# Kernel optimization log

Hardware: AMD Instinct MI355X
Metric: run time of the kernel (lower is better)

Reference implementation:

```python
import jax, jax.numpy as jnp
import numpy as np

B, IN_DIM, HID, K, D = 16384, 1024, 2048, 8192, 128
COMMIT = 0.25


def setup_inputs() -> dict:
    key = jax.random.key(0)
    ks = jax.random.split(key, 10)
    s1 = 1.0 / np.sqrt(IN_DIM)
    s2 = 1.0 / np.sqrt(HID)
    s3 = 1.0 / np.sqrt(D)
    return {
        "x": jax.random.uniform(ks[0], (B, IN_DIM), dtype=jnp.float32),
        "W1": jax.random.normal(ks[1], (IN_DIM, HID), dtype=jnp.float32) * s1,
        "b1": jnp.zeros((HID,), jnp.float32),
        "W2": jax.random.normal(ks[2], (HID, D), dtype=jnp.float32) * s2,
        "b2": jnp.zeros((D,), jnp.float32),
        # torch init: uniform(-1/K, 1/K)
        "codebook": jax.random.uniform(ks[3], (K, D), dtype=jnp.float32, minval=-1.0 / K, maxval=1.0 / K),
        "W3": jax.random.normal(ks[4], (D, HID), dtype=jnp.float32) * s3,
        "b3": jnp.zeros((HID,), jnp.float32),
        "W4": jax.random.normal(ks[5], (HID, IN_DIM), dtype=jnp.float32) * s2,
        "b4": jnp.zeros((IN_DIM,), jnp.float32),
    }


def reference(x, W1, b1, W2, b2, codebook, W3, b3, W4, b4):
    # Encoder MLP: [B, IN] -> [B, D]
    h = jax.nn.relu(x @ W1 + b1)
    z = h @ W2 + b2                                   # [B, D]

    # Squared-distance to codebook: ||z||^2 - 2 z C^T + ||C||^2  -> [B, K]
    dists = (jnp.sum(z * z, axis=1, keepdims=True)
             - 2.0 * (z @ codebook.T)
             + jnp.sum(codebook * codebook, axis=1))
    indices = jnp.argmin(dists, axis=1)               # [B]
    z_q = codebook[indices]                            # [B, D]

    # Straight-through estimator
    z_q_st = z + jax.lax.stop_gradient(z_q - z)

    # Decoder MLP: [B, D] -> [B, IN]
    h2 = jax.nn.relu(z_q_st @ W3 + b3)
    recon = jax.nn.sigmoid(h2 @ W4 + b4)

    sg_zq = jax.lax.stop_gradient(z_q)
    mse = jnp.mean(jnp.square(sg_zq - z))
    loss = mse + COMMIT * mse
    return (recon, loss, indices)
```

## Files before the change

### kernel.cpp

```cpp
#include <hip/hip_runtime.h>
#include <hip/hip_bf16.h>


#define B_    16384
#define INDIM 1024
#define HID   2048
#define KCB   8192
#define DDIM  128

#define CAND_CAP 2000000u
#define LBUF_CAP 1024u

typedef __bf16    bf16x8   __attribute__((ext_vector_type(8)));
typedef float     floatx4  __attribute__((ext_vector_type(4)));
typedef double    doublex4 __attribute__((ext_vector_type(4)));
typedef _Float16  half8    __attribute__((ext_vector_type(8)));
typedef __fp16    fp16x2   __attribute__((ext_vector_type(2)));

#define XS 4096.0f
#define WS 8192.0f
#define SCALE_INV 2.9802322387695312e-08

__device__ __forceinline__ unsigned long long pack_key(float d, int code)
{
    unsigned int u = __float_as_uint(d);
    u = (u & 0x80000000u) ? ~u : (u | 0x80000000u);
    return ((unsigned long long)u << 32) | (unsigned int)code;
}

__device__ __forceinline__ float unpack_d(unsigned long long key)
{
    unsigned int u = (unsigned int)(key >> 32);
    u = (u & 0x80000000u) ? (u ^ 0x80000000u) : ~u;
    return __uint_as_float(u);
}

__device__ __forceinline__ void gll16(const float* g, float* l)
{
    __builtin_amdgcn_global_load_lds(
        (const __attribute__((address_space(1))) void*)g,
        (__attribute__((address_space(3))) void*)l, 16, 0, 0);
}

template <int ACT, int PMASK>
__launch_bounds__(256)
__global__ void gemm_split_f16(const float* __restrict__ A, const _Float16* __restrict__ Bs_g,
                               const float* __restrict__ bias, float* __restrict__ Cout,
                               int M, int N, int K)
{
    __shared__ float    As[128 * 32];
    __shared__ _Float16 Bsh[64 * 64];

    const int t    = threadIdx.x;
    const int m0   = blockIdx.y * 128, n0 = blockIdx.x * 64;
    const int wave = t >> 6, lane = t & 63;
    const int wr   = (wave >> 1) * 64, wc = (wave & 1) * 32;
    const int quad = lane >> 4, l16 = lane & 15;
    const int lr   = lane >> 3;
    const int lcA  = ((lane & 7) ^ lr) * 4;
    const int slB  = lane & 7;
    const int lrB  = lane >> 3;

    floatx4  accf[4][2];
    doublex4 accd[4][2];
#pragma unroll
    for (int i = 0; i < 4; ++i)
#pragma unroll
        for (int j = 0; j < 2; ++j) {
            accf[i][j] = (floatx4){0.f, 0.f, 0.f, 0.f};
            accd[i][j] = (doublex4){0.0, 0.0, 0.0, 0.0};
        }

    const int NKT = K >> 5;
    for (int kt = 0; kt < NKT; ++kt) {
        const int k0 = kt << 5;
        __syncthreads();
#pragma unroll
        for (int s = 0; s < 4; ++s) {
            int r = wave * 32 + s * 8;
            gll16(A + (size_t)(m0 + r + lr) * K + k0 + lcA, &As[r * 32]);
        }
#pragma unroll
        for (int s = 0; s < 2; ++s) {
            int rb = wave * 16 + s * 8 + lrB;
            int ccs = slB ^ (lrB & 7);
            gll16((const float*)(Bs_g + (size_t)(n0 + rb) * (2 * K) + kt * 64 + ccs * 8),
                  (float*)&Bsh[(wave * 16 + s * 8) * 64]);
        }
        __syncthreads();

        half8 a1[4], a2[4];
#pragma unroll
        for (int i = 0; i < 4; ++i) {
            const int row = wr + i * 16 + l16;
            const int s0  = (2 * quad) ^ (row & 7);
            const int s1  = (2 * quad + 1) ^ (row & 7);
            floatx4 f0 = *(const floatx4*)&As[row * 32 + s0 * 4];
            floatx4 f1 = *(const floatx4*)&As[row * 32 + s1 * 4];
            union { half8 v; fp16x2 h[4]; } u1, u2;
            float sv[8];
#pragma unroll
            for (int q = 0; q < 4; ++q) sv[q] = f0[q] * XS;
#pragma unroll
            for (int q = 0; q < 4; ++q) sv[4 + q] = f1[q] * XS;
#pragma unroll
            for (int q = 0; q < 4; ++q) {
                fp16x2 hi = __builtin_amdgcn_cvt_pkrtz(sv[2 * q], sv[2 * q + 1]);
                u1.h[q] = hi;
                float r0 = sv[2 * q] - (float)hi[0];
                float r1 = sv[2 * q + 1] - (float)hi[1];
                u2.h[q] = __builtin_amdgcn_cvt_pkrtz(r0, r1);
            }
            a1[i] = u1.v; a2[i] = u2.v;
        }
        half8 b1[2], b2[2];
#pragma unroll
        for (int j = 0; j < 2; ++j) {
            const int row = wc + j * 16 + l16;
            b1[j] = *(const half8*)&Bsh[row * 64 + ((0 + quad) ^ (row & 7)) * 8];
            b2[j] = *(const half8*)&Bsh[row * 64 + ((4 + quad) ^ (row & 7)) * 8];
        }
#pragma unroll
        for (int i = 0; i < 4; ++i)
#pragma unroll
            for (int j = 0; j < 2; ++j)
                accf[i][j] = __builtin_amdgcn_mfma_f32_16x16x32_f16(a1[i], b1[j], accf[i][j], 0, 0, 0);
#pragma unroll
        for (int i = 0; i < 4; ++i)
#pragma unroll
            for (int j = 0; j < 2; ++j)
                accf[i][j] = __builtin_amdgcn_mfma_f32_16x16x32_f16(a1[i], b2[j], accf[i][j], 0, 0, 0);
#pragma unroll
        for (int i = 0; i < 4; ++i)
#pragma unroll
            for (int j = 0; j < 2; ++j)
                accf[i][j] = __builtin_amdgcn_mfma_f32_16x16x32_f16(a2[i], b1[j], accf[i][j], 0, 0, 0);

        if ((kt & PMASK) == PMASK) {
#pragma unroll
            for (int i = 0; i < 4; ++i)
#pragma unroll
                for (int j = 0; j < 2; ++j) {
#pragma unroll
                    for (int r = 0; r < 4; ++r)
                        accd[i][j][r] += (double)accf[i][j][r] * SCALE_INV;
                    accf[i][j] = (floatx4){0.f, 0.f, 0.f, 0.f};
                }
        }
    }
    if (NKT & PMASK) {
#pragma unroll
        for (int i = 0; i < 4; ++i)
#pragma unroll
            for (int j = 0; j < 2; ++j)
#pragma unroll
                for (int r = 0; r < 4; ++r)
                    accd[i][j][r] += (double)accf[i][j][r] * SCALE_INV;
    }

#pragma unroll
    for (int i = 0; i < 4; ++i)
#pragma unroll
        for (int j = 0; j < 2; ++j)
#pragma unroll
            for (int r = 0; r < 4; ++r) {
                int row = m0 + wr + i * 16 + quad * 4 + r;
                int col = n0 + wc + j * 16 + l16;
                float f = (float)(accd[i][j][r] + (double)bias[col]);
                if (ACT == 1) f = fmaxf(f, 0.f);
                Cout[(size_t)row * N + col] = f;
            }
}

template <int IM, int ACT, int PMASK, int SPLITOUT>
__launch_bounds__(256)
__global__ void gemm_split_pre(const _Float16* __restrict__ As_g, const _Float16* __restrict__ Bs_g,
                               const float* __restrict__ bias, void* __restrict__ Cp,
                               int M, int N, int K)
{
    __shared__ _Float16 Ash[IM * 32 * 64];
    __shared__ _Float16 Bsh[64 * 64];

    const int t    = threadIdx.x;
    const int nwg  = gridDim.x * gridDim.y;
    int lin = blockIdx.y * gridDim.x + blockIdx.x;
    lin = (lin & 7) * (nwg >> 3) + (lin >> 3);
    const int bx = lin % gridDim.x, by = lin / gridDim.x;
    const int m0   = by * (IM * 32), n0 = bx * 64;
    const int wave = t >> 6, lane = t & 63;
    const int wr   = (wave >> 1) * (IM * 16), wc = (wave & 1) * 32;
    const int quad = lane >> 4, l16 = lane & 15;
    const int slB  = lane & 7;
    const int lrB  = lane >> 3;
    const int ccs  = slB ^ (lrB & 7);

    floatx4  accf[IM][2];
    doublex4 accd[IM][2];
#pragma unroll
    for (int i = 0; i < IM; ++i)
#pragma unroll
        for (int j = 0; j < 2; ++j) {
            accf[i][j] = (floatx4){0.f, 0.f, 0.f, 0.f};
            accd[i][j] = (doublex4){0.0, 0.0, 0.0, 0.0};
        }

    const int NKT = K >> 5;
    for (int kt = 0; kt < NKT; ++kt) {
        __syncthreads();
#pragma unroll
        for (int s = 0; s < IM; ++s) {
            int ra = wave * (IM * 8) + s * 8 + lrB;
            gll16((const float*)(As_g + (size_t)(m0 + ra) * (2 * K) + kt * 64 + ccs * 8),
                  (float*)&Ash[(wave * (IM * 8) + s * 8) * 64]);
        }
#pragma unroll
        for (int s = 0; s < 2; ++s) {
            int rb = wave * 16 + s * 8 + lrB;
            gll16((const float*)(Bs_g + (size_t)(n0 + rb) * (2 * K) + kt * 64 + ccs * 8),
                  (float*)&Bsh[(wave * 16 + s * 8) * 64]);
        }
        __syncthreads();

        half8 a1[IM], a2[IM], b1[2], b2[2];
#pragma unroll
        for (int i = 0; i < IM; ++i) {
            const int row = wr + i * 16 + l16;
            a1[i] = *(const half8*)&Ash[row * 64 + ((0 + quad) ^ (row & 7)) * 8];
            a2[i] = *(const half8*)&Ash[row * 64 + ((4 + quad) ^ (row & 7)) * 8];
        }
#pragma unroll
        for (int j = 0; j < 2; ++j) {
            const int row = wc + j * 16 + l16;
            b1[j] = *(const half8*)&Bsh[row * 64 + ((0 + quad) ^ (row & 7)) * 8];
            b2[j] = *(const half8*)&Bsh[row * 64 + ((4 + quad) ^ (row & 7)) * 8];
        }
#pragma unroll
        for (int i = 0; i < IM; ++i)
#pragma unroll
            for (int j = 0; j < 2; ++j)
                accf[i][j] = __builtin_amdgcn_mfma_f32_16x16x32_f16(a1[i], b1[j], accf[i][j], 0, 0, 0);
#pragma unroll
        for (int i = 0; i < IM; ++i)
#pragma unroll
            for (int j = 0; j < 2; ++j)
                accf[i][j] = __builtin_amdgcn_mfma_f32_16x16x32_f16(a1[i], b2[j], accf[i][j], 0, 0, 0);
#pragma unroll
        for (int i = 0; i < IM; ++i)
#pragma unroll
            for (int j = 0; j < 2; ++j)
                accf[i][j] = __builtin_amdgcn_mfma_f32_16x16x32_f16(a2[i], b1[j], accf[i][j], 0, 0, 0);

        if ((kt & PMASK) == PMASK) {
#pragma unroll
            for (int i = 0; i < IM; ++i)
#pragma unroll
                for (int j = 0; j < 2; ++j) {
#pragma unroll
                    for (int r = 0; r < 4; ++r)
                        accd[i][j][r] += (double)accf[i][j][r] * SCALE_INV;
                    accf[i][j] = (floatx4){0.f, 0.f, 0.f, 0.f};
                }
        }
    }
    if (NKT & PMASK) {
#pragma unroll
        for (int i = 0; i < IM; ++i)
#pragma unroll
            for (int j = 0; j < 2; ++j)
#pragma unroll
                for (int r = 0; r < 4; ++r)
                    accd[i][j][r] += (double)accf[i][j][r] * SCALE_INV;
    }

#pragma unroll
    for (int i = 0; i < IM; ++i)
#pragma unroll
        for (int j = 0; j < 2; ++j)
#pragma unroll
            for (int r = 0; r < 4; ++r) {
                int row = m0 + wr + i * 16 + quad * 4 + r;
                int col = n0 + wc + j * 16 + l16;
                float f = (float)(accd[i][j][r] + (double)bias[col]);
                if (ACT == 1) f = fmaxf(f, 0.f);
                if (SPLITOUT == 1) {
                    float sv = f * XS;
                    _Float16 p0 = (_Float16)sv;
                    _Float16 p1 = (_Float16)(sv - (float)p0);
                    _Float16* hs = (_Float16*)Cp;
                    size_t base = (size_t)row * (2 * (size_t)N)
                                + (size_t)(col >> 5) * 64 + (col & 31);
                    hs[base]      = p0;
                    hs[base + 32] = p1;
                } else {
                    ((float*)Cp)[(size_t)row * N + col] = f;
                }
            }
}

template <int ACT>
__launch_bounds__(256)
__global__ void gemm_bf16_gll(const __bf16* __restrict__ A, const __bf16* __restrict__ BT,
                              const float* __restrict__ bias, void* __restrict__ Cp,
                              int M, int N, int K)
{
    __shared__ __bf16 Asm[128 * 32];
    __shared__ __bf16 Bsm[128 * 32];

    const int t    = threadIdx.x;
    const int nwg  = gridDim.x * gridDim.y;
    int lin = blockIdx.y * gridDim.x + blockIdx.x;
    lin = (lin & 7) * (nwg >> 3) + (lin >> 3);
    const int bx = lin % gridDim.x, by = lin / gridDim.x;
    const int m0   = by * 128, n0 = bx * 128;
    const int wave = t >> 6, lane = t & 63;
    const int wr   = (wave >> 1) * 64, wc = (wave & 1) * 64;
    const int quad = lane >> 4, l16 = lane & 15;
    const int srow = lane >> 2;
    const int schk = lane & 3;

    floatx4 acc[4][4];
#pragma unroll
    for (int i = 0; i < 4; ++i)
#pragma unroll
        for (int j = 0; j < 4; ++j) acc[i][j] = (floatx4){0.f, 0.f, 0.f, 0.f};

    for (int k0 = 0; k0 < K; k0 += 32) {
        __syncthreads();
#pragma unroll
        for (int s = 0; s < 2; ++s) {
            const int rbase = wave * 32 + s * 16;
            const int ra = rbase + srow;
            const int cs = (schk - (ra >> 1)) & 3;
            gll16((const float*)(A + (size_t)(m0 + ra) * K + k0 + cs * 8),
                  (float*)&Asm[rbase * 32]);
        }
#pragma unroll
        for (int s = 0; s < 2; ++s) {
            const int rbase = wave * 32 + s * 16;
            const int rb = rbase + srow;
            const int cs = (schk - (rb >> 1)) & 3;
            gll16((const float*)(BT + (size_t)(n0 + rb) * K + k0 + cs * 8),
                  (float*)&Bsm[rbase * 32]);
        }
        __syncthreads();

        bf16x8 af[4], bfr[4];
#pragma unroll
        for (int i = 0; i < 4; ++i) {
            const int rl = wr + i * 16 + l16;
            const int sl = (quad + (rl >> 1)) & 3;
            af[i] = *(const bf16x8*)&Asm[rl * 32 + sl * 8];
        }
#pragma unroll
        for (int j = 0; j < 4; ++j) {
            const int rl = wc + j * 16 + l16;
            const int sl = (quad + (rl >> 1)) & 3;
            bfr[j] = *(const bf16x8*)&Bsm[rl * 32 + sl * 8];
        }
#pragma unroll
        for (int i = 0; i < 4; ++i)
#pragma unroll
            for (int j = 0; j < 4; ++j)
                acc[i][j] = __builtin_amdgcn_mfma_f32_16x16x32_bf16(af[i], bfr[j], acc[i][j], 0, 0, 0);
    }

#pragma unroll
    for (int i = 0; i < 4; ++i)
#pragma unroll
        for (int j = 0; j < 4; ++j) {
            int col = n0 + wc + j * 16 + l16;
            float b = bias[col];
#pragma unroll
            for (int r = 0; r < 4; ++r) {
                int row = m0 + wr + i * 16 + quad * 4 + r;
                float v = acc[i][j][r] + b;
                if (ACT == 1) {
                    v = fmaxf(v, 0.f);
                    ((__bf16*)Cp)[(size_t)row * N + col] = (__bf16)v;
                } else {
                    v = 1.f / (1.f + __expf(-v));
                    ((float*)Cp)[(size_t)row * N + col] = v;
                }
            }
        }
}

__global__ void split_x(const float* __restrict__ in, _Float16* __restrict__ outS, int n8)
{
    int i = blockIdx.x * 256 + threadIdx.x;
    if (i >= n8) return;
    const int K = INDIM;
    int m  = i / (K / 8);
    int k8 = i % (K / 8);
    int k  = k8 * 8;
    const float* src = in + (size_t)m * K + k;
    floatx4 f0 = *(const floatx4*)(src);
    floatx4 f1 = *(const floatx4*)(src + 4);
    union { half8 v; fp16x2 h[4]; } u1, u2;
    float sv[8];
#pragma unroll
    for (int q = 0; q < 4; ++q) sv[q] = f0[q] * XS;
#pragma unroll
    for (int q = 0; q < 4; ++q) sv[4 + q] = f1[q] * XS;
#pragma unroll
    for (int q = 0; q < 4; ++q) {
        fp16x2 hi = __builtin_amdgcn_cvt_pkrtz(sv[2 * q], sv[2 * q + 1]);
        u1.h[q] = hi;
        float r0 = sv[2 * q] - (float)hi[0];
        float r1 = sv[2 * q + 1] - (float)hi[1];
        u2.h[q] = __builtin_amdgcn_cvt_pkrtz(r0, r1);
    }
    size_t base = (size_t)m * (2 * K) + (size_t)(k >> 5) * 64 + (k & 31);
    *(half8*)(outS + base)      = u1.v;
    *(half8*)(outS + base + 32) = u2.v;
}

__global__ void transpose_split_f16(const float* __restrict__ in, _Float16* __restrict__ outS,
                                    int K, int N)
{
    __shared__ float tile[32][33];
    int k0 = blockIdx.x * 32, n0 = blockIdx.y * 32;
    int tr = threadIdx.x >> 5, tc = threadIdx.x & 31;
#pragma unroll
    for (int s = 0; s < 4; ++s)
        tile[tr + 8 * s][tc] = in[(size_t)(k0 + tr + 8 * s) * N + n0 + tc];
    __syncthreads();
#pragma unroll
    for (int s = 0; s < 4; ++s) {
        int n = n0 + tr + 8 * s;
        int k = k0 + tc;
        float w = tile[tc][tr + 8 * s] * WS;
        _Float16 p0 = (_Float16)w;
        float r = w - (float)p0;
        _Float16 p1 = (_Float16)r;
        size_t base = (size_t)n * (2 * K) + (size_t)(k >> 5) * 64 + (k & 31);
        outS[base]      = p0;
        outS[base + 32] = p1;
    }
}

__global__ void rownorm_kernel(const float* __restrict__ M, float* __restrict__ nrm)
{
    int k = blockIdx.x * 4 + (threadIdx.x >> 6);
    int lane = threadIdx.x & 63;
    float2 c = *(const float2*)(M + (size_t)k * DDIM + lane * 2);
    float q0 = c.x * c.x;
    float q1 = c.y * c.y;
    double s = (double)q0 + (double)q1;
#pragma unroll
    for (int off = 32; off > 0; off >>= 1) s += __shfl_down(s, off);
    if (lane == 0) nrm[k] = (float)s;
}

__global__ void cnmax_kernel(const float* __restrict__ cn, float* __restrict__ out)
{
    __shared__ float red[4];
    int t = threadIdx.x;
    float m = 0.f;
    for (int i = t; i < KCB; i += 256) m = fmaxf(m, cn[i]);
#pragma unroll
    for (int off = 32; off > 0; off >>= 1) m = fmaxf(m, __shfl_down(m, off));
    if ((t & 63) == 0) red[t >> 6] = m;
    __syncthreads();
    if (t == 0) out[0] = fmaxf(fmaxf(red[0], red[1]), fmaxf(red[2], red[3]));
}

__global__ void cvt_half(const float* __restrict__ in, _Float16* __restrict__ out,
                         float scale, int n8)
{
    int i = blockIdx.x * 256 + threadIdx.x;
    if (i >= n8) return;
    const float4 a = *(const float4*)(in + (size_t)i * 8);
    const float4 b = *(const float4*)(in + (size_t)i * 8 + 4);
    half8 h;
    h[0] = (_Float16)(a.x * scale); h[1] = (_Float16)(a.y * scale);
    h[2] = (_Float16)(a.z * scale); h[3] = (_Float16)(a.w * scale);
    h[4] = (_Float16)(b.x * scale); h[5] = (_Float16)(b.y * scale);
    h[6] = (_Float16)(b.z * scale); h[7] = (_Float16)(b.w * scale);
    *(half8*)(out + (size_t)i * 8) = h;
}

template <int EMIT>
__launch_bounds__(256)
__global__ void score_sweep2(const _Float16* __restrict__ zh, const _Float16* __restrict__ ch,
                             const float* __restrict__ nz32, const float* __restrict__ cn32,
                             unsigned long long* __restrict__ gbestA,
                             const float* __restrict__ cnmaxp,
                             unsigned* __restrict__ listCnt, unsigned* __restrict__ list)
{
    __shared__ __align__(16) _Float16 Zs[32 * 128];
    __shared__ __align__(16) _Float16 Cs[128 * 128];
    __shared__ unsigned long long best[32];
    __shared__ unsigned lbuf[LBUF_CAP];
    __shared__ unsigned lcnt, lbase;

    const int t    = threadIdx.x;
    int bid = blockIdx.x;
    bid = (bid & 7) * ((int)gridDim.x >> 3) + (bid >> 3);
    const int m0   = bid * 32;
    const int wave = t >> 6, lane = t & 63;
    const int quad = lane >> 4, l16 = lane & 15;
    const int srow = lane >> 4, sc = lane & 15;

    if (EMIT == 0) { if (t < 32) best[t] = ~0ull; }
    else if (t == 0) lcnt = 0u;

#pragma unroll
    for (int s = 0; s < 2; ++s) {
        const int rbase = s * 16 + wave * 4;
        const int ra = rbase + srow;
        const int cs = sc ^ ((ra & 7) << 1);
        gll16((const float*)(zh + (size_t)(m0 + ra) * 128 + cs * 8),
              (float*)&Zs[rbase * 128]);
    }
    __syncthreads();

    half8 af[2][4];
#pragma unroll
    for (int i = 0; i < 2; ++i) {
        const int rl = i * 16 + l16;
#pragma unroll
        for (int ks = 0; ks < 4; ++ks) {
            const int cc = (ks * 4 + quad) ^ ((rl & 7) << 1);
            af[i][ks] = *(const half8*)&Zs[rl * 128 + cc * 8];
        }
    }

    const float cnm = *cnmaxp;
    float nzv[8], thr[8], bd[8];
    int   bc[8];
#pragma unroll
    for (int i = 0; i < 2; ++i)
#pragma unroll
        for (int r = 0; r < 4; ++r) {
            const int q = i * 4 + r;
            const int grow = m0 + i * 16 + quad * 4 + r;
            nzv[q] = nz32[grow];
            if (EMIT) {
                thr[q] = unpack_d(gbestA[grow]) + 2.4e-3f * sqrtf(nzv[q] * cnm) + 6.0e-5f;
            } else {
                bd[q] = 3.4e38f; bc[q] = 0x7fffffff;
            }
        }

    for (int nt = 0; nt < KCB / 128; ++nt) {
        const int n0 = nt * 128;
        __syncthreads();
#pragma unroll
        for (int s = 0; s < 8; ++s) {
            const int rbase = s * 16 + wave * 4;
            const int ra = rbase + srow;
            const int cs = sc ^ ((ra & 7) << 1);
            gll16((const float*)(ch + (size_t)(n0 + ra) * 128 + cs * 8),
                  (float*)&Cs[rbase * 128]);
        }
        float cnj[2];
#pragma unroll
        for (int j = 0; j < 2; ++j)
            cnj[j] = cn32[n0 + wave * 32 + j * 16 + l16];
        __syncthreads();

        floatx4 acc[2][2];
#pragma unroll
        for (int i = 0; i < 2; ++i)
#pragma unroll
            for (int j = 0; j < 2; ++j) acc[i][j] = (floatx4){0.f, 0.f, 0.f, 0.f};
#pragma unroll
        for (int ks = 0; ks < 4; ++ks) {
            half8 bf[2];
#pragma unroll
            for (int j = 0; j < 2; ++j) {
                const int rl = wave * 32 + j * 16 + l16;
                const int cc = (ks * 4 + quad) ^ ((rl & 7) << 1);
                bf[j] = *(const half8*)&Cs[rl * 128 + cc * 8];
            }
#pragma unroll
            for (int i = 0; i < 2; ++i)
#pragma unroll
                for (int j = 0; j < 2; ++j)
                    acc[i][j] = __builtin_amdgcn_mfma_f32_16x16x32_f16(af[i][ks], bf[j], acc[i][j], 0, 0, 0);
        }

#pragma unroll
        for (int i = 0; i < 2; ++i)
#pragma unroll
            for (int r = 0; r < 4; ++r) {
                const int q = i * 4 + r;
#pragma unroll
                for (int j = 0; j < 2; ++j) {
                    const int code = n0 + wave * 32 + j * 16 + l16;
                    float s = acc[i][j][r] * (1.0f / 4096.0f);
                    float d = (nzv[q] - 2.0f * s) + cnj[j];
                    if (EMIT) {
                        if (d <= thr[q]) {
                            unsigned ent = ((unsigned)(m0 + i * 16 + quad * 4 + r) << 13) | (unsigned)code;
                            unsigned idx = atomicAdd(&lcnt, 1u);
                            if (idx < LBUF_CAP) lbuf[idx] = ent;
                            else {
                                unsigned g = atomicAdd(listCnt, 1u);
                                if (g < CAND_CAP) list[g] = ent;
                            }
                        }
                    } else {
                        if (d < bd[q]) { bd[q] = d; bc[q] = code; }
                    }
                }
            }
    }

    if (EMIT == 0) {
#pragma unroll
        for (int i = 0; i < 2; ++i)
#pragma unroll
            for (int r = 0; r < 4; ++r) {
                const int q = i * 4 + r;
                atomicMin(&best[i * 16 + quad * 4 + r], pack_key(bd[q], bc[q]));
            }
        __syncthreads();
        if (t < 32) gbestA[m0 + t] = best[t];
    } else {
        __syncthreads();
        unsigned cnt = lcnt; if (cnt > LBUF_CAP) cnt = LBUF_CAP;
        if (t == 0) lbase = atomicAdd(listCnt, cnt);
        __syncthreads();
        for (unsigned e = t; e < cnt; e += 256) {
            unsigned g = lbase + e;
            if (g < CAND_CAP) list[g] = lbuf[e];
        }
    }
}

__launch_bounds__(256)
__global__ void refine_kernel(const float* __restrict__ z, const float* __restrict__ cb,
                              const float* __restrict__ nz32, const float* __restrict__ cn32,
                              const unsigned* __restrict__ listCnt,
                              const unsigned* __restrict__ list,
                              unsigned long long* __restrict__ gbest)
{
    unsigned cnt = *listCnt;
    if (cnt > CAND_CAP) cnt = CAND_CAP;
    const int lane = threadIdx.x & 63;
    for (unsigned p = blockIdx.x * 4 + (threadIdx.x >> 6); p < cnt; p += gridDim.x * 4) {
        const unsigned e = list[p];
        const int r = (int)(e >> 13), k = (int)(e & 8191u);
        float2 zv = *(const float2*)(z  + (size_t)r * DDIM + lane * 2);
        float2 cv = *(const float2*)(cb + (size_t)k * DDIM + lane * 2);
        double s = (double)zv.x * (double)cv.x + (double)zv.y * (double)cv.y;
#pragma unroll
        for (int off = 32; off > 0; off >>= 1) s += __shfl_down(s, off);
        if (lane == 0) {
            float s32 = (float)s;
            float d = (nz32[r] - 2.0f * s32) + cn32[k];
            atomicMin(&gbest[r], pack_key(d, k));
        }
    }
}

__global__ void init_gbest(unsigned long long* __restrict__ g,
                           double* __restrict__ acc, unsigned* __restrict__ cnt)
{
    g[blockIdx.x * 256 + threadIdx.x] = ~0ull;
    if (blockIdx.x == 0 && threadIdx.x == 0) { *acc = 0.0; *cnt = 0u; }
}

__global__ void gather_zq_loss(const float* __restrict__ z, const float* __restrict__ cb,
                               const unsigned long long* __restrict__ gbest,
                               __bf16* __restrict__ zqb, double* __restrict__ acc)
{
    int r = blockIdx.x * 4 + (threadIdx.x >> 6);
    int lane = threadIdx.x & 63;
    int k = (int)(gbest[r] & 0xffffffffull);
    float2 zv = *(const float2*)(z  + (size_t)r * DDIM + lane * 2);
    float2 cv = *(const float2*)(cb + (size_t)k * DDIM + lane * 2);
    __bf16 b0 = (__bf16)cv.x, b1 = (__bf16)cv.y;
    zqb[(size_t)r * DDIM + lane * 2]     = b0;
    zqb[(size_t)r * DDIM + lane * 2 + 1] = b1;
    double dx = (double)cv.x - (double)zv.x, dy = (double)cv.y - (double)zv.y;
    double s = dx * dx + dy * dy;
#pragma unroll
    for (int off = 32; off > 0; off >>= 1) s += __shfl_down(s, off);
    if (lane == 0) atomicAdd(acc, s);
}

__global__ void finalize_kernel(const unsigned long long* __restrict__ gbest,
                                const double* __restrict__ acc, float* __restrict__ out)
{
    int tid = blockIdx.x * 256 + threadIdx.x;
    if (tid < B_) out[16777217 + tid] = (float)(int)(gbest[tid] & 0xffffffffull);
    if (tid == 0) out[16777216] = (float)((*acc) * 1.25 / (double)(B_ * DDIM));
}

__global__ void transpose_to_bf16(const float* __restrict__ in, __bf16* __restrict__ outT,
                                  int K, int N)
{
    __shared__ float tile[32][33];
    int k0 = blockIdx.x * 32, n0 = blockIdx.y * 32;
    int tr = threadIdx.x >> 5, tc = threadIdx.x & 31;
#pragma unroll
    for (int s = 0; s < 4; ++s)
        tile[tr + 8 * s][tc] = in[(size_t)(k0 + tr + 8 * s) * N + n0 + tc];
    __syncthreads();
#pragma unroll
    for (int s = 0; s < 4; ++s)
        outT[(size_t)(n0 + tr + 8 * s) * K + k0 + tc] = (__bf16)tile[tc][tr + 8 * s];
}

extern "C" void kernel_launch(void* const* d_in, const int* in_sizes, int n_in,
                              void* d_out, int out_size, void* d_ws, size_t ws_size,
                              hipStream_t stream)
{
    const float* x  = (const float*)d_in[0];
    const float* W1 = (const float*)d_in[1];
    const float* b1 = (const float*)d_in[2];
    const float* W2 = (const float*)d_in[3];
    const float* b2 = (const float*)d_in[4];
    const float* cb = (const float*)d_in[5];
    const float* W3 = (const float*)d_in[6];
    const float* b3 = (const float*)d_in[7];
    const float* W4 = (const float*)d_in[8];
    const float* b4 = (const float*)d_in[9];
    float* out = (float*)d_out;

    char* ws = (char*)d_ws;
    _Float16* hs = (_Float16*)(ws);
    float*  h    = (float*)(ws);
    __bf16* h2b  = (__bf16*)(ws + 16777216ull);
    _Float16* zh  = (_Float16*)(ws);
    _Float16* chh = (_Float16*)(ws + 4194304ull);
    unsigned long long* gbestA = (unsigned long long*)(ws + 6291456ull);
    unsigned* list = (unsigned*)(ws + 8388608ull);
    float*  z32  = (float*)(ws + 134217728ull);
    __bf16* zqb  = (__bf16*)(ws + 142606336ull);
    _Float16* W1s = (_Float16*)(ws + 142606336ull);
    float*  nz32 = (float*)(ws + 150994944ull);
    float*  cn32 = (float*)(ws + 151060480ull);
    unsigned long long* gbest = (unsigned long long*)(ws + 151093248ull);
    double* acc  = (double*)(ws + 151224320ull);
    float*  cnmax   = (float*)(ws + 151224328ull);
    unsigned* listCnt = (unsigned*)(ws + 151224332ull);
    __bf16* W3t  = (__bf16*)(ws + 151228416ull);
    __bf16* W4t  = (__bf16*)(ws + 151752704ull);
    _Float16* W2s = (_Float16*)(ws + 155947008ull);

    const unsigned long long XS_OFF = 157286400ull;
    _Float16* xs = (_Float16*)(ws + XS_OFF);
    const bool pre_split_x = (ws_size >= XS_OFF + 67108864ull);

    init_gbest<<<B_ / 256, 256, 0, stream>>>(gbest, acc, listCnt);
    rownorm_kernel<<<KCB / 4, 256, 0, stream>>>(cb, cn32);
    cnmax_kernel<<<1, 256, 0, stream>>>(cn32, cnmax);
    transpose_to_bf16<<<dim3(DDIM / 32, HID / 32), 256, 0, stream>>>(W3, W3t, DDIM, HID);
    transpose_to_bf16<<<dim3(HID / 32, INDIM / 32), 256, 0, stream>>>(W4, W4t, HID, INDIM);
    transpose_split_f16<<<dim3(INDIM / 32, HID / 32), 256, 0, stream>>>(W1, W1s, INDIM, HID);
    transpose_split_f16<<<dim3(HID / 32, DDIM / 32), 256, 0, stream>>>(W2, W2s, HID, DDIM);

    if (pre_split_x) {
        split_x<<<(B_ * INDIM / 8) / 256, 256, 0, stream>>>(x, xs, B_ * INDIM / 8);
        gemm_split_pre<4, 1, 3, 1><<<dim3(HID / 64, B_ / 128), 256, 0, stream>>>(
            xs, W1s, b1, (void*)hs, B_, HID, INDIM);
        gemm_split_pre<2, 0, 1, 0><<<dim3(DDIM / 64, B_ / 64), 256, 0, stream>>>(
            hs, W2s, b2, (void*)z32, B_, DDIM, HID);
    } else {
        gemm_split_f16<1, 3><<<dim3(HID / 64, B_ / 128), 256, 0, stream>>>(
            x, W1s, b1, h, B_, HID, INDIM);
        gemm_split_f16<0, 1><<<dim3(DDIM / 64, B_ / 128), 256, 0, stream>>>(
            h, W2s, b2, z32, B_, DDIM, HID);
    }
    rownorm_kernel<<<B_ / 4, 256, 0, stream>>>(z32, nz32);

    cvt_half<<<(B_ * DDIM / 8) / 256, 256, 0, stream>>>(z32, zh, 1.0f, B_ * DDIM / 8);
    cvt_half<<<(KCB * DDIM / 8) / 256, 256, 0, stream>>>(cb, chh, 4096.0f, KCB * DDIM / 8);
    score_sweep2<0><<<B_ / 32, 256, 0, stream>>>(
        zh, chh, nz32, cn32, gbestA, cnmax, listCnt, list);
    score_sweep2<1><<<B_ / 32, 256, 0, stream>>>(
        zh, chh, nz32, cn32, gbestA, cnmax, listCnt, list);
    refine_kernel<<<1024, 256, 0, stream>>>(z32, cb, nz32, cn32, listCnt, list, gbest);

    gather_zq_loss<<<B_ / 4, 256, 0, stream>>>(z32, cb, gbest, zqb, acc);
    gemm_bf16_gll<1><<<dim3(HID / 128, B_ / 128), 256, 0, stream>>>(
        zqb, W3t, b3, (void*)h2b, B_, HID, DDIM);
    gemm_bf16_gll<2><<<dim3(INDIM / 128, B_ / 128), 256, 0, stream>>>(
        h2b, W4t, b4, (void*)out, B_, INDIM, HID);

    finalize_kernel<<<B_ / 256, 256, 0, stream>>>(gbest, acc, out);
}
```

Baseline: 944.1 us.

## Fuse two-pass codebook sweep into a single pass with running row-min threshold

Replaces the separate min-finding sweep and candidate-emitting sweep with one kernel. Each tile computes distances, updates a shared per-row running minimum via LDS atomicMin, syncs, then emits candidates within a margin of the current running minimum. This removes a full second codebook GEMM sweep and the global best-key buffer. In exchange it adds an extra barrier and LDS atomics per tile. Early tiles use looser thresholds, so more candidates reach the refine kernel.

```diff
diff --git a/kernel.cpp b/kernel.cpp
--- a/kernel.cpp
+++ b/kernel.cpp
@@ -28,10 +28,14 @@
     return ((unsigned long long)u << 32) | (unsigned int)code;
 }
 
-__device__ __forceinline__ float unpack_d(unsigned long long key)
-{
-    unsigned int u = (unsigned int)(key >> 32);
-    u = (u & 0x80000000u) ? (u ^ 0x80000000u) : ~u;
+__device__ __forceinline__ unsigned packf(float d)
+{
+    unsigned u = __float_as_uint(d);
+    return (u & 0x80000000u) ? ~u : (u | 0x80000000u);
+}
+__device__ __forceinline__ float unpackf(unsigned p)
+{
+    unsigned u = (p & 0x80000000u) ? (p ^ 0x80000000u) : ~p;
     return __uint_as_float(u);
 }
 
@@ -480,17 +484,15 @@
     *(half8*)(out + (size_t)i * 8) = h;
 }
 
-template <int EMIT>
 __launch_bounds__(256)
-__global__ void score_sweep2(const _Float16* __restrict__ zh, const _Float16* __restrict__ ch,
+__global__ void score_sweep3(const _Float16* __restrict__ zh, const _Float16* __restrict__ ch,
                              const float* __restrict__ nz32, const float* __restrict__ cn32,
-                             unsigned long long* __restrict__ gbestA,
                              const float* __restrict__ cnmaxp,
                              unsigned* __restrict__ listCnt, unsigned* __restrict__ list)
 {
     __shared__ __align__(16) _Float16 Zs[32 * 128];
     __shared__ __align__(16) _Float16 Cs[128 * 128];
-    __shared__ unsigned long long best[32];
+    __shared__ unsigned rowmin[32];
     __shared__ unsigned lbuf[LBUF_CAP];
     __shared__ unsigned lcnt, lbase;
 
@@ -502,8 +504,8 @@
     const int quad = lane >> 4, l16 = lane & 15;
     const int srow = lane >> 4, sc = lane & 15;
 
-    if (EMIT == 0) { if (t < 32) best[t] = ~0ull; }
-    else if (t == 0) lcnt = 0u;
+    if (t == 0) lcnt = 0u;
+    if (t < 32) rowmin[t] = 0xFFFFFFFFu;
 
 #pragma unroll
     for (int s = 0; s < 2; ++s) {
@@ -527,20 +529,19 @@
     }
 
     const float cnm = *cnmaxp;
-    float nzv[8], thr[8], bd[8];
-    int   bc[8];
+    float nzv[8], W[8];
+    unsigned cachemin[8];
+    int rowidx[8];
 #pragma unroll
     for (int i = 0; i < 2; ++i)
 #pragma unroll
         for (int r = 0; r < 4; ++r) {
             const int q = i * 4 + r;
-            const int grow = m0 + i * 16 + quad * 4 + r;
+            rowidx[q] = i * 16 + quad * 4 + r;
+            const int grow = m0 + rowidx[q];
             nzv[q] = nz32[grow];
-            if (EMIT) {
-                thr[q] = unpack_d(gbestA[grow]) + 2.4e-3f * sqrtf(nzv[q] * cnm) + 6.0e-5f;
-            } else {
-                bd[q] = 3.4e38f; bc[q] = 0x7fffffff;
-            }
+            W[q]   = 2.4e-3f * sqrtf(nzv[q] * cnm) + 6.0e-5f;
+            cachemin[q] = 0xFFFFFFFFu;
         }
 
     for (int nt = 0; nt < KCB / 128; ++nt) {
@@ -581,6 +582,7 @@
                     acc[i][j] = __builtin_amdgcn_mfma_f32_16x16x32_f16(af[i][ks], bf[j], acc[i][j], 0, 0, 0);
         }
 
+        float dv[8][2];
 #pragma unroll
         for (int i = 0; i < 2; ++i)
 #pragma unroll
@@ -588,45 +590,46 @@
                 const int q = i * 4 + r;
 #pragma unroll
                 for (int j = 0; j < 2; ++j) {
-                    const int code = n0 + wave * 32 + j * 16 + l16;
                     float s = acc[i][j][r] * (1.0f / 4096.0f);
-                    float d = (nzv[q] - 2.0f * s) + cnj[j];
-                    if (EMIT) {
-                        if (d <= thr[q]) {
-                            unsigned ent = ((unsigned)(m0 + i * 16 + quad * 4 + r) << 13) | (unsigned)code;
-                            unsigned idx = atomicAdd(&lcnt, 1u);
-                            if (idx < LBUF_CAP) lbuf[idx] = ent;
-                            else {
-                                unsigned g = atomicAdd(listCnt, 1u);
-                                if (g < CAND_CAP) list[g] = ent;
-                            }
+                    dv[q][j] = (nzv[q] - 2.0f * s) + cnj[j];
+                }
+                unsigned lp = packf(fminf(dv[q][0], dv[q][1]));
+                if (lp < cachemin[q])
+                    atomicMin(&rowmin[rowidx[q]], lp);
+            }
+        __syncthreads();
+
+#pragma unroll
+        for (int i = 0; i < 2; ++i)
+#pragma unroll
+            for (int r = 0; r < 4; ++r) {
+                const int q = i * 4 + r;
+                unsigned rp = rowmin[rowidx[q]];
+                cachemin[q] = rp;
+                const float thr = unpackf(rp) + W[q];
+#pragma unroll
+                for (int j = 0; j < 2; ++j) {
+                    if (dv[q][j] <= thr) {
+                        const int code = n0 + wave * 32 + j * 16 + l16;
+                        unsigned ent = ((unsigned)(m0 + rowidx[q]) << 13) | (unsigned)code;
+                        unsigned idx = atomicAdd(&lcnt, 1u);
+                        if (idx < LBUF_CAP) lbuf[idx] = ent;
+                        else {
+                            unsigned g = atomicAdd(listCnt, 1u);
+                            if (g < CAND_CAP) list[g] = ent;
                         }
-                    } else {
-                        if (d < bd[q]) { bd[q] = d; bc[q] = code; }
                     }
                 }
             }
     }
 
-    if (EMIT == 0) {
-#pragma unroll
-        for (int i = 0; i < 2; ++i)
-#pragma unroll
-            for (int r = 0; r < 4; ++r) {
-                const int q = i * 4 + r;
-                atomicMin(&best[i * 16 + quad * 4 + r], pack_key(bd[q], bc[q]));
-            }
-        __syncthreads();
-        if (t < 32) gbestA[m0 + t] = best[t];
-    } else {
-        __syncthreads();
-        unsigned cnt = lcnt; if (cnt > LBUF_CAP) cnt = LBUF_CAP;
-        if (t == 0) lbase = atomicAdd(listCnt, cnt);
-        __syncthreads();
-        for (unsigned e = t; e < cnt; e += 256) {
-            unsigned g = lbase + e;
-            if (g < CAND_CAP) list[g] = lbuf[e];
-        }
+    __syncthreads();
+    unsigned cnt = lcnt; if (cnt > LBUF_CAP) cnt = LBUF_CAP;
+    if (t == 0) lbase = atomicAdd(listCnt, cnt);
+    __syncthreads();
+    for (unsigned e = t; e < cnt; e += 256) {
+        unsigned g = lbase + e;
+        if (g < CAND_CAP) list[g] = lbuf[e];
     }
 }
 
@@ -727,7 +730,6 @@
     __bf16* h2b  = (__bf16*)(ws + 16777216ull);
     _Float16* zh  = (_Float16*)(ws);
     _Float16* chh = (_Float16*)(ws + 4194304ull);
-    unsigned long long* gbestA = (unsigned long long*)(ws + 6291456ull);
     unsigned* list = (unsigned*)(ws + 8388608ull);
     float*  z32  = (float*)(ws + 134217728ull);
     __bf16* zqb  = (__bf16*)(ws + 142606336ull);
@@ -770,10 +772,8 @@
 
     cvt_half<<<(B_ * DDIM / 8) / 256, 256, 0, stream>>>(z32, zh, 1.0f, B_ * DDIM / 8);
     cvt_half<<<(KCB * DDIM / 8) / 256, 256, 0, stream>>>(cb, chh, 4096.0f, KCB * DDIM / 8);
-    score_sweep2<0><<<B_ / 32, 256, 0, stream>>>(
-        zh, chh, nz32, cn32, gbestA, cnmax, listCnt, list);
-    score_sweep2<1><<<B_ / 32, 256, 0, stream>>>(
-        zh, chh, nz32, cn32, gbestA, cnmax, listCnt, list);
+    score_sweep3<<<B_ / 32, 256, 0, stream>>>(
+        zh, chh, nz32, cn32, cnmax, listCnt, list);
     refine_kernel<<<1024, 256, 0, stream>>>(z32, cb, nz32, cn32, listCnt, list, gbest);
 
     gather_zq_loss<<<B_ / 4, 256, 0, stream>>>(z32, cb, gbest, zqb, acc);
```

Measured after the change: 947.1 us. Within noise of the previous version (+0.3%).
